# Kernel optimization log

Measured on AMD Instinct MI355X. Metric: run time of the kernel, lower is better.

The kernel has to match this reference:

```python
import jax, jax.numpy as jnp
import numpy as np

B, D = 8192, 2048

def setup_inputs() -> dict:
    key = jax.random.key(0)
    ks = jax.random.split(key, 6)
    names = ["head_real", "head_imag", "rel_real", "rel_imag", "tail_real", "tail_imag"]
    return {n: jax.random.normal(k, (B, D), dtype=jnp.float32) for n, k in zip(names, ks)}

def reference(head_real, head_imag, rel_real, rel_imag, tail_real, tail_imag):
    # Complex rotation of head by rel (note sign convention of the original code):
    #   rot_real = hr*rr - hi*ri ; rot_imag = -(hi*rr + hr*ri)
    rot_real = head_real * rel_real - head_imag * rel_imag
    rot_imag = -(head_imag * rel_real + head_real * rel_imag)
    # Original computes full [B, D, D] matmuls then extracts trace via einsum('bii->b').
    # trace(A @ B^T) == sum of elementwise products -> compute the reduction directly.
    ab = jnp.sum(rot_real * tail_real + rot_imag * tail_imag, axis=1)   # [B]
    aa = jnp.sum(rot_real * rot_real + rot_imag * rot_imag, axis=1)     # [B]
    bb = jnp.sum(tail_real * tail_real + tail_imag * tail_imag, axis=1) # [B]
    return ab / jnp.sqrt(aa * bb)
```

## Files before the change

kernel.cpp:

```cpp
#include <hip/hip_runtime.h>


#define BLOCK 256
#define DCOLS 2048

__global__ __launch_bounds__(BLOCK) void chrono_rot_kernel(
    const float* __restrict__ hr, const float* __restrict__ hi,
    const float* __restrict__ rr, const float* __restrict__ ri,
    const float* __restrict__ tr, const float* __restrict__ ti,
    float* __restrict__ out)
{
    const int row = blockIdx.x;
    const int t   = threadIdx.x;
    const size_t base = (size_t)row * DCOLS;

    const float4* hr4 = (const float4*)(hr + base);
    const float4* hi4 = (const float4*)(hi + base);
    const float4* rr4 = (const float4*)(rr + base);
    const float4* ri4 = (const float4*)(ri + base);
    const float4* tr4 = (const float4*)(tr + base);
    const float4* ti4 = (const float4*)(ti + base);

    float s_ab = 0.f, s_aa = 0.f, s_bb = 0.f;

    #pragma unroll
    for (int it = 0; it < DCOLS / (BLOCK * 4); ++it) {
        const int i = it * BLOCK + t;
        const float4 a = hr4[i];
        const float4 b = hi4[i];
        const float4 c = rr4[i];
        const float4 d = ri4[i];
        const float4 e = tr4[i];
        const float4 f = ti4[i];

        #pragma unroll
        for (int j = 0; j < 4; ++j) {
            const float av = (&a.x)[j], bv = (&b.x)[j];
            const float cv = (&c.x)[j], dv = (&d.x)[j];
            const float ev = (&e.x)[j], fv = (&f.x)[j];
            const float rot_r = av * cv - bv * dv;
            const float rot_i = -(bv * cv + av * dv);
            s_ab += rot_r * ev + rot_i * fv;
            s_aa += rot_r * rot_r + rot_i * rot_i;
            s_bb += ev * ev + fv * fv;
        }
    }

    #pragma unroll
    for (int off = 32; off > 0; off >>= 1) {
        s_ab += __shfl_down(s_ab, off, 64);
        s_aa += __shfl_down(s_aa, off, 64);
        s_bb += __shfl_down(s_bb, off, 64);
    }

    __shared__ float red[3][BLOCK / 64];
    const int wave = t >> 6;
    const int lane = t & 63;
    if (lane == 0) {
        red[0][wave] = s_ab;
        red[1][wave] = s_aa;
        red[2][wave] = s_bb;
    }
    __syncthreads();
    if (t == 0) {
        float ab = 0.f, aa = 0.f, bb = 0.f;
        #pragma unroll
        for (int w = 0; w < BLOCK / 64; ++w) {
            ab += red[0][w];
            aa += red[1][w];
            bb += red[2][w];
        }
        out[row] = ab / sqrtf(aa * bb);
    }
}

extern "C" void kernel_launch(void* const* d_in, const int* in_sizes, int n_in,
                              void* d_out, int out_size, void* d_ws, size_t ws_size,
                              hipStream_t stream) {
    const float* hr = (const float*)d_in[0];
    const float* hi = (const float*)d_in[1];
    const float* rr = (const float*)d_in[2];
    const float* ri = (const float*)d_in[3];
    const float* tr = (const float*)d_in[4];
    const float* ti = (const float*)d_in[5];
    float* out = (float*)d_out;

    const int B = out_size;
    chrono_rot_kernel<<<B, BLOCK, 0, stream>>>(hr, hi, rr, ri, tr, ti, out);
}
```

Before: 328.8 us.

## Assign one wave per row and software-prefetch the next chunk

Each 64-lane wave now reduces a whole row, so the block-level shared-memory reduction and barrier are gone and four rows run per block. The loop loads the next chunk of six float4 values while the current one is being computed, a form of register double-buffering meant to keep more loads in flight. In exchange each thread runs more iterations (8 instead of 2) and needs more registers. The kernel reads a large amount of data, so it is mostly memory-bound and the gain depends on whether memory-level parallelism gets better.

```diff
diff --git a/kernel.cpp b/kernel.cpp
--- a/kernel.cpp
+++ b/kernel.cpp
@@ -3,6 +3,8 @@
 
 #define BLOCK 256
 #define DCOLS 2048
+#define WAVES_PER_BLOCK (BLOCK / 64)
+#define CHUNKS (DCOLS / 4 / 64)
 
 __global__ __launch_bounds__(BLOCK) void chrono_rot_kernel(
     const float* __restrict__ hr, const float* __restrict__ hi,
@@ -10,40 +12,47 @@
     const float* __restrict__ tr, const float* __restrict__ ti,
     float* __restrict__ out)
 {
-    const int row = blockIdx.x;
-    const int t   = threadIdx.x;
+    const int wave = threadIdx.x >> 6;
+    const int lane = threadIdx.x & 63;
+    const int row  = blockIdx.x * WAVES_PER_BLOCK + wave;
     const size_t base = (size_t)row * DCOLS;
 
-    const float4* hr4 = (const float4*)(hr + base);
-    const float4* hi4 = (const float4*)(hi + base);
-    const float4* rr4 = (const float4*)(rr + base);
-    const float4* ri4 = (const float4*)(ri + base);
-    const float4* tr4 = (const float4*)(tr + base);
-    const float4* ti4 = (const float4*)(ti + base);
+    const float4* __restrict__ hr4 = (const float4*)(hr + base);
+    const float4* __restrict__ hi4 = (const float4*)(hi + base);
+    const float4* __restrict__ rr4 = (const float4*)(rr + base);
+    const float4* __restrict__ ri4 = (const float4*)(ri + base);
+    const float4* __restrict__ tr4 = (const float4*)(tr + base);
+    const float4* __restrict__ ti4 = (const float4*)(ti + base);
 
     float s_ab = 0.f, s_aa = 0.f, s_bb = 0.f;
 
+    int i = lane;
+    float4 a0 = hr4[i], b0 = hi4[i], c0 = rr4[i],
+           d0 = ri4[i], e0 = tr4[i], f0 = ti4[i];
+
     #pragma unroll
-    for (int it = 0; it < DCOLS / (BLOCK * 4); ++it) {
-        const int i = it * BLOCK + t;
-        const float4 a = hr4[i];
-        const float4 b = hi4[i];
-        const float4 c = rr4[i];
-        const float4 d = ri4[i];
-        const float4 e = tr4[i];
-        const float4 f = ti4[i];
+    for (int it = 0; it < CHUNKS; ++it) {
+        float4 a1, b1, c1, d1, e1, f1;
+        if (it + 1 < CHUNKS) {
+            const int j = i + 64;
+            a1 = hr4[j]; b1 = hi4[j]; c1 = rr4[j];
+            d1 = ri4[j]; e1 = tr4[j]; f1 = ti4[j];
+        }
 
         #pragma unroll
-        for (int j = 0; j < 4; ++j) {
-            const float av = (&a.x)[j], bv = (&b.x)[j];
-            const float cv = (&c.x)[j], dv = (&d.x)[j];
-            const float ev = (&e.x)[j], fv = (&f.x)[j];
+        for (int k = 0; k < 4; ++k) {
+            const float av = (&a0.x)[k], bv = (&b0.x)[k];
+            const float cv = (&c0.x)[k], dv = (&d0.x)[k];
+            const float ev = (&e0.x)[k], fv = (&f0.x)[k];
             const float rot_r = av * cv - bv * dv;
             const float rot_i = -(bv * cv + av * dv);
             s_ab += rot_r * ev + rot_i * fv;
             s_aa += rot_r * rot_r + rot_i * rot_i;
             s_bb += ev * ev + fv * fv;
         }
+
+        a0 = a1; b0 = b1; c0 = c1; d0 = d1; e0 = e1; f0 = f1;
+        i += 64;
     }
 
     #pragma unroll
@@ -53,24 +62,8 @@
         s_bb += __shfl_down(s_bb, off, 64);
     }
 
-    __shared__ float red[3][BLOCK / 64];
-    const int wave = t >> 6;
-    const int lane = t & 63;
     if (lane == 0) {
-        red[0][wave] = s_ab;
-        red[1][wave] = s_aa;
-        red[2][wave] = s_bb;
-    }
-    __syncthreads();
-    if (t == 0) {
-        float ab = 0.f, aa = 0.f, bb = 0.f;
-        #pragma unroll
-        for (int w = 0; w < BLOCK / 64; ++w) {
-            ab += red[0][w];
-            aa += red[1][w];
-            bb += red[2][w];
-        }
-        out[row] = ab / sqrtf(aa * bb);
+        out[row] = s_ab / sqrtf(s_aa * s_bb);
     }
 }
 
@@ -86,5 +79,5 @@
     float* out = (float*)d_out;
 
     const int B = out_size;
-    chrono_rot_kernel<<<B, BLOCK, 0, stream>>>(hr, hi, rr, ri, tr, ti, out);
+    chrono_rot_kernel<<<B / WAVES_PER_BLOCK, BLOCK, 0, stream>>>(hr, hi, rr, ri, tr, ti, out);
 }
```

After: 340.0 us. 1.03x slower.
